# Performance work log

Hardware: AMD Instinct MI355X
Metric: run time of the kernel (lower is better)

Reference implementation:

```python
import jax, jax.numpy as jnp
import numpy as np

P, Q = 8, 8  # patch_size


def _patchify(x):
    # x: [b, c, H, W] -> patches [b, h*w, c*p*q]
    b, c, H, W = x.shape
    h, w = H // P, W // Q
    x = x.reshape(b, c, h, P, w, Q)
    x = x.transpose(0, 2, 4, 1, 3, 5)  # b h w c p q
    return x.reshape(b, h * w, c * P * Q)


def _depatchify(patches, c, H, W):
    # patches: [b, h*w, c*p*q] -> [b, c, H, W]
    b = patches.shape[0]
    h, w = H // P, W // Q
    x = patches.reshape(b, h, w, c, P, Q)
    x = x.transpose(0, 3, 1, 4, 2, 5)  # b c h p w q
    return x.reshape(b, c, H, W)


def setup_inputs() -> dict:
    key = jax.random.key(0)
    x = jax.random.normal(key, (16, 3, 512, 512), dtype=jnp.float32)
    return {"x": x, "rank": 32}


def reference(x, rank):
    b, c, H, W = x.shape
    patches = _patchify(x)  # [b, N, D] with N = (H/8)*(W/8), D = c*64
    u, s, vt = jnp.linalg.svd(patches, full_matrices=False)
    u = u[..., :rank]          # [b, N, r]
    s = s[..., :rank]          # [b, r]
    vt = vt[..., :rank, :]     # [b, r, D]
    # original: u*sqrt(s), v = sqrt(s)*vt^T; reconstruction u @ v^T == (u*s) @ vt
    recon = (u * s[..., None, :]) @ vt  # [b, N, D]
    return _depatchify(recon, c, H, W)
```

## Files before the change

### kernel.cpp

```cpp
#include <hip/hip_runtime.h>
#include <cstdint>
#include <cstddef>

#define IMG 512
#define JD 192

__device__ inline float fast_rcp(float x) { return __builtin_amdgcn_rcpf(x); }

__global__ __launch_bounds__(256) void k_gram(const float* __restrict__ x,
                                              float* __restrict__ part) {
  const int ck = blockIdx.x;
  const int sl = blockIdx.y;
  const int b  = blockIdx.z;
  const int t  = threadIdx.x;
  __shared__ float tile[32][JD];
  const int ty = t >> 5;
  const int tx = t & 31;
  const int r0 = sl*48 + ty*6;
  const int c0 = tx*6;
  float acc[6][6];
#pragma unroll
  for (int i=0;i<6;i++)
#pragma unroll
    for (int j=0;j<6;j++) acc[i][j]=0.f;
// ... 69 lines not shown
      const int row = f >> 5, kk = f & 31;
      Ar[row][kk] = Sb[(ti*64+row)*JD + k0+kk];
      Br[row][kk] = Sb[(tj*64+row)*JD + k0+kk];
    }
    __syncthreads();
#pragma unroll 4
    for (int k=0;k<32;k++) {
      float va[4], vb[4];
#pragma unroll
      for (int i=0;i<4;i++) va[i] = Ar[ty*4+i][k];
#pragma unroll
      for (int j=0;j<4;j++) vb[j] = Br[tx*4+j][k];
#pragma unroll
      for (int i=0;i<4;i++)
#pragma unroll
        for (int j=0;j<4;j++) acc[i][j] += va[i]*vb[j];
    }
    __syncthreads();
  }
#pragma unroll
  for (int i=0;i<4;i++)
#pragma unroll
    for (int j=0;j<4;j++) {
      const int r = ti*64+ty*4+i, c = tj*64+tx*4+j;
      Db[r*JD+c] = acc[i][j];
      if (ti != tj) Db[c*JD+r] = acc[i][j];
    }
}


__device__ void orth_lds(float* __restrict__ Wl, float* __restrict__ S1,
                         float* __restrict__ rdv, float* __restrict__ pdv,
                         float* __restrict__ misc, int t, float ridge) {
  const int ty = t >> 4, tx = t & 15;
  float acc[4][4];
#pragma unroll
  for (int i=0;i<4;i++)
#pragma unroll
    for (int j=0;j<4;j++) acc[i][j]=0.f;
  __syncthreads();
#pragma unroll 2
  for (int r=0; r<JD; r++) {
    const float4 va4 = *(const float4*)(Wl + r*68 + ty*4);
    const float4 vb4 = *(const float4*)(Wl + r*68 + tx*4);
    const float a4[4] = {va4.x, va4.y, va4.z, va4.w};
    const float b4[4] = {vb4.x, vb4.y, vb4.z, vb4.w};
#pragma unroll
    for (int i=0;i<4;i++)
#pragma unroll
      for (int j=0;j<4;j++) acc[i][j] += a4[i]*b4[j];
  }
#pragma unroll
  for (int i=0;i<4;i++)
#pragma unroll
    for (int j=0;j<4;j++)
      S1[(ty*4+i)*68 + tx*4+j] = acc[i][j];
  __syncthreads();
  if (ridge > 0.f) {
    if (t < 64) {
      float d = S1[t*68+t];
#pragma unroll
      for (int o=1;o<64;o<<=1) d = fmaxf(d, __shfl_xor(d, o));
      if (t == 0) misc[0] = d * ridge;
    }
    __syncthreads();
    if (t < 64) S1[t*68+t] += misc[0];
    __syncthreads();
  }
  for (int p=0; p<4; p++) {
    const int b16 = p*16;
    if (t < 64) {
      for (int jj=0; jj<16; jj++) {
        const int j = b16 + jj;
        const float invd = fast_rcp(S1[j*68+j]);
        if (t == 0) pdv[jj] = invd;
        const int nit = (15-jj)*16;
        for (int f=t; f<nit; f+=64) {
          const int i = j+1 + (f>>4);
          const int k = j+1 + (f&15);
          if (k <= i)
            S1[i*68+k] -= S1[i*68+j]*S1[k*68+j]*invd;
        }
      }
    }
    __syncthreads();
    const int rb = b16 + 16;
    if (t < 64 - rb) {
      const int r = rb + t;
      float pr[16];
      float4* prp = (float4*)pr;
      prp[0] = *(const float4*)(S1 + r*68 + b16);
      prp[1] = *(const float4*)(S1 + r*68 + b16 + 4);
      prp[2] = *(const float4*)(S1 + r*68 + b16 + 8);
      prp[3] = *(const float4*)(S1 + r*68 + b16 + 12);
#pragma unroll
      for (int c=1; c<16; c++) {
        float s = pr[c];
#pragma unroll
        for (int j=0; j<c; j++) s -= pr[j]*S1[(b16+c)*68 + b16+j]*pdv[j];
        pr[c] = s;
      }
      *(float4*)(S1 + r*68 + b16)      = prp[0];
      *(float4*)(S1 + r*68 + b16 + 4)  = prp[1];
      *(float4*)(S1 + r*68 + b16 + 8)  = prp[2];
      *(float4*)(S1 + r*68 + b16 + 12) = prp[3];
    }
    __syncthreads();
    for (int f=t; f<2304; f+=256) {
      const int i = rb + f/48;
      const int k = rb + (f - (f/48)*48);
      if (i < 64 && k < 64 && k <= i) {
        float s = S1[i*68+k];
#pragma unroll
        for (int jj=0; jj<16; jj++)
          s -= S1[i*68 + b16+jj]*S1[k*68 + b16+jj]*pdv[jj];
        S1[i*68+k] = s;
      }
    }
    __syncthreads();
  }
  if (t < 64) rdv[t] = rsqrtf(S1[t*68+t]);
  __syncthreads();
  for (int f=t; f<4096; f+=256) {
    const int i = f>>6, k = f&63;
    if (k < i) S1[i*68+k] *= rdv[k];
  }
  __syncthreads();
  if (t < JD) {
    float w[64];
    float4* wp = (float4*)w;
#pragma unroll
    for (int c4=0;c4<16;c4++) wp[c4] = *(const float4*)(Wl + t*68 + c4*4);
#pragma unroll
    for (int c=0;c<64;c++) {
      float v = w[c];
#pragma unroll
      for (int k=0;k<c;k++) v -= w[k]*S1[c*68+k];
      w[c] = v * rdv[c];
    }
#pragma unroll
    for (int c4=0;c4<16;c4++) *(float4*)(Wl + t*68 + c4*4) = wp[c4];
  }
  __syncthreads();
}

__device__ void mm_lds(const float* __restrict__ G, const float* __restrict__ Win,
                       float* __restrict__ Wout, float* __restrict__ Gt, int t) {
  const int rg = t >> 2, cg = t & 3;
  float acc[3][16];
#pragma unroll
  for (int i=0;i<3;i++)
#pragma unroll
    for (int j=0;j<16;j++) acc[i][j]=0.f;
  for (int k0=0; k0<JD; k0+=32) {
    __syncthreads();
    for (int f=t; f<6144; f+=256) {
      const int r = f >> 5, kk = f & 31;
      Gt[kk*193 + r] = G[r*JD + k0 + kk];
    }
    __syncthreads();
#pragma unroll 2
    for (int k=0;k<32;k++) {
      const float a0 = Gt[k*193 + rg*3+0];
      const float a1 = Gt[k*193 + rg*3+1];
      const float a2 = Gt[k*193 + rg*3+2];
      const float* wr = Win + (k0+k)*68 + cg*16;
#pragma unroll
      for (int j4=0;j4<4;j4++) {
        const float4 b4 = *(const float4*)(wr + 4*j4);
        const float bb[4] = {b4.x, b4.y, b4.z, b4.w};
#pragma unroll
        for (int jj=0;jj<4;jj++) {
          acc[0][j4*4+jj] += a0*bb[jj];
          acc[1][j4*4+jj] += a1*bb[jj];
          acc[2][j4*4+jj] += a2*bb[jj];
        }
      }
    }
  }
  __syncthreads();
#pragma unroll
  for (int i=0;i<3;i++)
#pragma unroll
    for (int j=0;j<16;j++)
      Wout[(rg*3+i)*68 + cg*16 + j] = acc[i][j];
  __syncthreads();
}

__device__ void hgemm_lds(const float* __restrict__ X, const float* __restrict__ Y,
                          float* __restrict__ S1, int t) {
  const int ty = t >> 4, tx = t & 15;
  float acc[4][4];
#pragma unroll
  for (int i=0;i<4;i++)
#pragma unroll
    for (int j=0;j<4;j++) acc[i][j]=0.f;
#pragma unroll 2
  for (int r=0; r<JD; r++) {
    const float4 va4 = *(const float4*)(X + r*68 + ty*4);
    const float4 vb4 = *(const float4*)(Y + r*68 + tx*4);
    const float a4[4] = {va4.x, va4.y, va4.z, va4.w};
    const float b4[4] = {vb4.x, vb4.y, vb4.z, vb4.w};
#pragma unroll
    for (int i=0;i<4;i++)
#pragma unroll
      for (int j=0;j<4;j++) acc[i][j] += a4[i]*b4[j];
  }
  __syncthreads();
#pragma unroll
  for (int i=0;i<4;i++)
#pragma unroll
    for (int j=0;j<4;j++)
      S1[(ty*4+i)*68 + tx*4+j] = acc[i][j];
  __syncthreads();
}

__global__ __launch_bounds__(256) void k_sub(const float* __restrict__ G32g,
                                             const float* __restrict__ Gsg,
                                             float* __restrict__ WbG,
                                             float* __restrict__ Hgg) {
  const int b = blockIdx.x;
  const int t = threadIdx.x;
  __shared__ float W0l[192*68];
  __shared__ float W1l[192*68];
  __shared__ float scr[32*193];
  __shared__ float rdv[64];
  __shared__ float pdv[16];
  __shared__ float misc[8];
  const float* Gb  = G32g + (size_t)b*JD*JD;
  const float* Gsb = Gsg  + (size_t)b*JD*JD;

  for (int f=t; f<JD*64; f+=256)
    W0l[(f>>6)*68 + (f&63)] = Gb[(f>>6)*JD + (f&63)];
  __syncthreads();

  orth_lds(W0l, scr, rdv, pdv, misc, t, 1e-6f);
  mm_lds(Gb, W0l, W1l, scr, t);
  orth_lds(W1l, scr, rdv, pdv, misc, t, 1e-6f);
  orth_lds(W1l, scr, rdv, pdv, misc, t, 0.f);

  mm_lds(Gsb, W1l, W0l, scr, t);
  hgemm_lds(W1l, W0l, scr, t);

  float* Wb = WbG + (size_t)b*JD*64;
  for (int f=t; f<JD*64; f+=256)
    Wb[f] = W1l[(f>>6)*68 + (f&63)];
  float* Hb = Hgg + (size_t)b*64*68;
  for (int f=t; f<64*68; f+=256) Hb[f] = scr[f];
}

__device__ void dev_tridiag(float* __restrict__ A, float* a, float* b2,
                            float* bsg, float* v0s, float* bts,
                            float* vvec, float* wvec, int t) {
  for (int j=0; j<=61; j++) {
    const int m = 63 - j;
    if (t < 64) {
      float xi = (t < m) ? A[j*68 + (j+1+t)] : 0.f;
      float nr = xi*xi;
#pragma unroll
      for (int o=1;o<64;o<<=1) nr += __shfl_xor(nr, o);
      const float sig = sqrtf(nr);
      const float alpha = __shfl(xi, 0);
      const float sgn = (alpha >= 0.f) ? 1.f : -1.f;
      const float v0 = alpha + sgn*sig;
      const float beta = (sig > 1e-20f) ? 1.0f/(sig*fabsf(v0)) : 0.f;
      if (t < m) vvec[t] = (t==0) ? v0 : xi;
      if (t == 0) {
        a[j] = A[j*68+j]; b2[j] = nr; bsg[j] = -sgn*sig;
        v0s[j] = v0; bts[j] = beta;
      }
      float pv = 0.f;
      if (t < m) {
        const float* row = A + (j+1+t)*68 + (j+1);
        for (int c=0;c<m;c++) pv += row[c]*vvec[c];
        pv *= beta;
      }
      float dp = (t<m) ? vvec[t]*pv : 0.f;
#pragma unroll
      for (int o=1;o<64;o<<=1) dp += __shfl_xor(dp, o);
      const float gamma = 0.5f*beta*dp;
      if (t < m) wvec[t] = pv - gamma*vvec[t];
    }
    __syncthreads();
    const int mm = m*m;
    for (int f=t; f<mm; f+=256) {
      const int r = f/m, c = f - r*m;
      A[(j+1+r)*68 + (j+1+c)] -= vvec[r]*wvec[c] + wvec[r]*vvec[c];
    }
    __syncthreads();
  }
  if (t == 0) {
    a[62] = A[62*68+62];
    a[63] = A[63*68+63];
    const float bb = A[62*68+63];
    b2[62] = bb*bb;
    bsg[62] = bb;
  }
  __syncthreads();
}

__device__ inline int sturm_cnt_fast(const float* a, const float* b2, float sig) {
  float d = a[0] - sig;
  int n = (d < 0.f) ? 1 : 0;
#pragma unroll 8
  for (int i=1;i<64;i++) {
    const float dd = (fabsf(d) < 1e-20f) ? -1e-20f : d;
    d = (a[i]-sig) - b2[i-1]*fast_rcp(dd);
    n += (d < 0.f) ? 1 : 0;
  }
  return n;
}

__device__ inline float dguard(float d) {
  if (fabsf(d) < 1e-12f) return (d < 0.f) ? -1e-12f : 1e-12f;
  return d;
}

__global__ __launch_bounds__(256) void k_tri(float* __restrict__ Hgg,
                                             float* __restrict__ vec5) {
  const int b = blockIdx.x;
  const int t = threadIdx.x;
  __shared__ float SH[64*68];
  __shared__ float a64[64];
  __shared__ float b2v[64];
  __shared__ float bsg[64];
  __shared__ float v0s[64];
  __shared__ float bts[64];
  __shared__ float vvec[64];
  __shared__ float wvec[64];
  float* Hb = Hgg + (size_t)b*64*68;
  for (int f=t; f<64*68; f+=256) SH[f] = Hb[f];
  __syncthreads();
  dev_tridiag(SH, a64, b2v, bsg, v0s, bts, vvec, wvec, t);
  for (int f=t; f<64*68; f+=256) Hb[f] = SH[f];
  float* vb = vec5 + (size_t)b*320;
  if (t < 64) {
    vb[t]     = a64[t];
    vb[64+t]  = b2v[t];
    vb[128+t] = bsg[t];
    vb[192+t] = v0s[t];
    vb[256+t] = bts[t];
  }
}

__global__ __launch_bounds__(256) void k_vec(const float* __restrict__ Hgg,
                                             const float* __restrict__ vec5,
                                             float* __restrict__ VtG) {
  const int b = blockIdx.x;
  const int t = threadIdx.x;
  __shared__ float SH[64*68];
  __shared__ float Vt[64*36];
  __shared__ float dpA[64*33];
  __shared__ float dmA[64*33];
  __shared__ float ps[8*33];
  __shared__ float wvred[32];
  __shared__ float rdv[64];
  __shared__ float a64[64];
  __shared__ float b2v[64];
  __shared__ float bsg[64];
  __shared__ float v0s[64];
  __shared__ float bts[64];
  __shared__ float lam[32];
  __shared__ float misc[8];
  const float* Hb = Hgg + (size_t)b*64*68;
  const float* vb = vec5 + (size_t)b*320;
  for (int f=t; f<64*68; f+=256) SH[f] = Hb[f];
  if (t < 64) {
    a64[t] = vb[t];
    b2v[t] = vb[64+t];
    bsg[t] = vb[128+t];
    v0s[t] = vb[192+t];
    bts[t] = vb[256+t];
  }
  __syncthreads();

  if (t < 64) {
    const float bl = (t>0)  ? sqrtf(b2v[t-1]) : 0.f;
    const float br = (t<63) ? sqrtf(b2v[t])   : 0.f;
    float lo = a64[t] - bl - br, hi = a64[t] + bl + br;
#pragma unroll
    for (int o=1;o<64;o<<=1) {
      lo = fminf(lo, __shfl_xor(lo,o));
      hi = fmaxf(hi, __shfl_xor(hi,o));
    }
    if (t == 0) { misc[0] = lo - 1e-4f; misc[1] = hi + 1e-4f; }
  }
  __syncthreads();

  {
    const int l = t >> 3, g = t & 7;
    const int r = 32 + l;
    float L = misc[0], H = misc[1];
    for (int it=0; it<10; it++) {
      const float mid = L + (H-L)*((float)(g+1)*(1.0f/9.0f));
      const int cnt = sturm_cnt_fast(a64, b2v, mid);
      float nL = L, nH = H;
#pragma unroll
      for (int k=0;k<8;k++) {
        const int ck = __shfl(cnt, k, 8);
        const float pk = L + (H-L)*((float)(k+1)*(1.0f/9.0f));
        if (ck <= r) nL = fmaxf(nL, pk); else nH = fminf(nH, pk);
      }
      L = nL; H = nH;
    }
    if (g == 0) lam[l] = 0.5f*(L+H);
  }
  __syncthreads();
// ... 62 lines not shown
        dpA[i*33+k] -= dpA[i*33+j]*dpA[k*33+j]*invd;
    }
  }
  __syncthreads();
  if (t < 32) rdv[t] = rsqrtf(dpA[t*33+t]);
  __syncthreads();
  for (int f=t; f<1024; f+=256) {
    const int i = f>>5, k = f&31;
    if (k < i) dpA[i*33+k] *= rdv[k];
  }
  __syncthreads();
  if (t < 64) {
    float w[32];
#pragma unroll
    for (int c=0;c<32;c++) w[c] = Vt[t*36+c];
#pragma unroll
    for (int c=0;c<32;c++) {
      float v = w[c];
#pragma unroll
      for (int k=0;k<c;k++) v -= w[k]*dpA[c*33+k];
      w[c] = v * rdv[c];
    }
#pragma unroll
    for (int c=0;c<32;c++) Vt[t*36+c] = w[c];
  }
  __syncthreads();

  for (int j=61; j>=0; j--) {
    const int m = 63 - j;
    {
      const int c = t & 31, g = t >> 5;
      float s = 0.f;
      for (int r=g; r<m; r+=8) {
        const float vr = (r==0) ? v0s[j] : SH[j*68 + (j+1+r)];
        s += vr * Vt[(j+1+r)*36 + c];
      }
      ps[g*33+c] = s;
    }
    __syncthreads();
    if (t < 32) {
      float s = 0.f;
#pragma unroll
      for (int g=0;g<8;g++) s += ps[g*33+t];
      wvred[t] = s * bts[j];
    }
    __syncthreads();
    {
      const int c = t & 31, g = t >> 5;
      for (int r=g; r<m; r+=8) {
        const float vr = (r==0) ? v0s[j] : SH[j*68 + (j+1+r)];
        Vt[(j+1+r)*36 + c] -= vr * wvred[c];
      }
    }
    __syncthreads();
  }

  float* Vb = VtG + (size_t)b*2048;
  for (int f=t; f<2048; f+=256) Vb[f] = Vt[(f>>5)*36 + (f&31)];
}

__global__ __launch_bounds__(256) void k_bm(const float* __restrict__ WbG,
                                            const float* __restrict__ VtG,
                                            float* __restrict__ Mg) {
  const int b = blockIdx.x;
  const int t = threadIdx.x;
  __shared__ float Vt[64*36];
  __shared__ float Bt[32*196];
  const float* W = WbG + (size_t)b*JD*64;
  const float* Vb = VtG + (size_t)b*2048;
  float* Mb = Mg + (size_t)b*JD*JD;
  for (int f=t; f<2048; f+=256) Vt[(f>>5)*36 + (f&31)] = Vb[f];
  __syncthreads();

  if (t < JD) {
    float accv[32];
#pragma unroll
    for (int c=0;c<32;c++) accv[c] = 0.f;
    const float4* crow = (const float4*)(W + t*64);
#pragma unroll 2
    for (int kb=0; kb<16; kb++) {
      const float4 av = crow[kb];
      const float a4[4] = {av.x, av.y, av.z, av.w};
#pragma unroll
      for (int ki=0; ki<4; ki++) {
        const float aa = a4[ki];
        const float* vrow = Vt + (kb*4+ki)*36;
        const float4 v0 = *(const float4*)(vrow+0);
        const float4 v1 = *(const float4*)(vrow+4);
        const float4 v2 = *(const float4*)(vrow+8);
        const float4 v3 = *(const float4*)(vrow+12);
        const float4 v4 = *(const float4*)(vrow+16);
        const float4 v5 = *(const float4*)(vrow+20);
        const float4 v6 = *(const float4*)(vrow+24);
        const float4 v7 = *(const float4*)(vrow+28);
        accv[0]+=aa*v0.x; accv[1]+=aa*v0.y; accv[2]+=aa*v0.z; accv[3]+=aa*v0.w;
        accv[4]+=aa*v1.x; accv[5]+=aa*v1.y; accv[6]+=aa*v1.z; accv[7]+=aa*v1.w;
        accv[8]+=aa*v2.x; accv[9]+=aa*v2.y; accv[10]+=aa*v2.z; accv[11]+=aa*v2.w;
        accv[12]+=aa*v3.x; accv[13]+=aa*v3.y; accv[14]+=aa*v3.z; accv[15]+=aa*v3.w;
        accv[16]+=aa*v4.x; accv[17]+=aa*v4.y; accv[18]+=aa*v4.z; accv[19]+=aa*v4.w;
        accv[20]+=aa*v5.x; accv[21]+=aa*v5.y; accv[22]+=aa*v5.z; accv[23]+=aa*v5.w;
        accv[24]+=aa*v6.x; accv[25]+=aa*v6.y; accv[26]+=aa*v6.z; accv[27]+=aa*v6.w;
        accv[28]+=aa*v7.x; accv[29]+=aa*v7.y; accv[30]+=aa*v7.z; accv[31]+=aa*v7.w;
      }
    }
#pragma unroll
    for (int c=0;c<32;c++) Bt[c*196 + t] = accv[c];
  }
  __syncthreads();

  for (int tt=t; tt<576; tt+=256) {
    const int tr = tt/24, tc = tt - tr*24;
    const int r0 = tr*8, c0 = tc*8;
    float acc2[8][8];
#pragma unroll
    for (int i=0;i<8;i++)
#pragma unroll
      for (int j=0;j<8;j++) acc2[i][j]=0.f;
    for (int k=0;k<32;k++) {
      const float* br = Bt + k*196;
      const float4 a0 = *(const float4*)(br + r0);
      const float4 a1 = *(const float4*)(br + r0 + 4);
      const float4 b0 = *(const float4*)(br + c0);
      const float4 b1 = *(const float4*)(br + c0 + 4);
      const float va[8] = {a0.x,a0.y,a0.z,a0.w,a1.x,a1.y,a1.z,a1.w};
      const float vb[8] = {b0.x,b0.y,b0.z,b0.w,b1.x,b1.y,b1.z,b1.w};
#pragma unroll
      for (int i=0;i<8;i++)
#pragma unroll
        for (int j=0;j<8;j++) acc2[i][j] += va[i]*vb[j];
    }
#pragma unroll
    for (int i=0;i<8;i++)
#pragma unroll
      for (int j=0;j<8;j++)
        Mb[(r0+i)*JD + c0+j] = acc2[i][j];
  }
}

__global__ __launch_bounds__(256) void k_recon(const float* __restrict__ x,
                                               const float* __restrict__ Mg,
                                               float* __restrict__ out) {
  const int nb = blockIdx.x;
  const int b  = blockIdx.y;
  const int t  = threadIdx.x;
  __shared__ float At[32][17];
  __shared__ float Mt[16][JD];
  const float* xb = x + (size_t)b*3*IMG*IMG;
  const float* Mb = Mg + (size_t)b*JD*JD;
  float* ob = out + (size_t)b*3*IMG*IMG;
  const int pg = t >> 4;
  const int jg = t & 15;
  float acc[2][12];
#pragma unroll
  for (int i=0;i<2;i++)
#pragma unroll
    for (int j=0;j<12;j++) acc[i][j]=0.f;
  for (int j0=0; j0<JD; j0+=16) {
    for (int f=t; f<512; f+=256) {
      const int nl = f >> 4, jj = f & 15;
      const int j = j0 + jj;
      const int n = nb*32 + nl;
      const int hh = n >> 6, ww = n & 63;
      const int c = j >> 6, p = (j >> 3) & 7, q = j & 7;
      At[nl][jj] = xb[(c*IMG + hh*8+p)*IMG + ww*8 + q];
    }
    for (int f=t; f<3072; f+=256) {
      const int jj = f / JD, cc = f - jj*JD;
      Mt[jj][cc] = Mb[(j0+jj)*JD + cc];
    }
    __syncthreads();
#pragma unroll 4
    for (int jj=0;jj<16;jj++) {
      const float a0 = At[pg*2+0][jj];
      const float a1 = At[pg*2+1][jj];
#pragma unroll
      for (int j=0;j<12;j++) {
        const float mm = Mt[jj][jg*12+j];
        acc[0][j] += a0*mm;
        acc[1][j] += a1*mm;
      }
    }
    __syncthreads();
  }
#pragma unroll
  for (int i=0;i<2;i++) {
    const int n = nb*32 + pg*2 + i;
    const int hh = n >> 6, ww = n & 63;
#pragma unroll
    for (int j4=0;j4<3;j4++) {
      const int jo = jg*12 + j4*4;
      const int c = jo >> 6, p = (jo >> 3) & 7, q = jo & 7;
      const float4 v = make_float4(acc[i][j4*4+0], acc[i][j4*4+1],
                                   acc[i][j4*4+2], acc[i][j4*4+3]);
      *(float4*)(ob + (size_t)(c*IMG + hh*8+p)*IMG + ww*8 + q) = v;
    }
  }
}

extern "C" void kernel_launch(void* const* d_in, const int* in_sizes, int n_in,
                              void* d_out, int out_size, void* d_ws, size_t ws_size,
                              hipStream_t stream) {
  (void)in_sizes; (void)n_in; (void)out_size; (void)ws_size;
  const float* x = (const float*)d_in[0];
  float* out = (float*)d_out;
  float* ws  = (float*)d_ws;

  float* part = ws;
  float* Gs   = ws + 2359296;
  float* P0   = ws + 2949120;
  float* P1   = ws + 3538944;
  float* Mg   = ws;
  float* Wb   = ws + 786432;
  float* Hg   = ws + 983040;
  float* v5   = ws + 1052672;
  float* Vtg  = ws + 1057792;

  k_gram  <<<dim3(4,4,16), 256, 0, stream>>>(x, part);
  k_greduce<<<2304,        256, 0, stream>>>(part, Gs);
  k_sq    <<<dim3(6,16),   256, 0, stream>>>(Gs, P0);
  k_sq    <<<dim3(6,16),   256, 0, stream>>>(P0, P1);
  k_sq    <<<dim3(6,16),   256, 0, stream>>>(P1, P0);
  k_sq    <<<dim3(6,16),   256, 0, stream>>>(P0, P1);
  k_sq    <<<dim3(6,16),   256, 0, stream>>>(P1, P0);
  k_sub   <<<16,           256, 0, stream>>>(P0, Gs, Wb, Hg);
  k_tri   <<<16,           256, 0, stream>>>(Hg, v5);
  k_vec   <<<16,           256, 0, stream>>>(Hg, v5, Vtg);
  k_bm    <<<16,           256, 0, stream>>>(Wb, Vtg, Mg);
  k_recon <<<dim3(128,16), 256, 0, stream>>>(x, Mg, out);
}
```

Before: 952.0 us.

## Widen k_sub to 1024 threads with smaller per-thread GEMM tiles

Launches the per-batch subspace-iteration kernel k_sub with 1024 threads instead of 256 and remaps its LDS GEMMs (Gram, mm, hgemm) to 2x2 or 3x4 per-thread tiles. Strided loops now step by 1024. The triangular-solve step of orth_lds now works directly on the LDS row instead of copying it into a 64-float register array. The goal is more parallelism in a kernel that runs only 16 blocks. The risks are less reuse per thread, more LDS traffic, and slower LDS access in the forward solve. Some sections, such as the Cholesky panel step guarded by t<64 and the t<JD solve, may not be written to use the extra threads.

Result: slower. 1.060 ms (+11.4%).

```diff
diff --git a/kernel.cpp b/kernel.cpp
--- a/kernel.cpp
+++ b/kernel.cpp
@@ -125,29 +125,20 @@
 __device__ void orth_lds(float* __restrict__ Wl, float* __restrict__ S1,
                          float* __restrict__ rdv, float* __restrict__ pdv,
                          float* __restrict__ misc, int t, float ridge) {
-  const int ty = t >> 4, tx = t & 15;
-  float acc[4][4];
-#pragma unroll
-  for (int i=0;i<4;i++)
-#pragma unroll
-    for (int j=0;j<4;j++) acc[i][j]=0.f;
-  __syncthreads();
-#pragma unroll 2
+  const int ty = t >> 5, tx = t & 31;
+  float a00=0.f, a01=0.f, a10=0.f, a11=0.f;
+  __syncthreads();
+#pragma unroll 4
   for (int r=0; r<JD; r++) {
-    const float4 va4 = *(const float4*)(Wl + r*68 + ty*4);
-    const float4 vb4 = *(const float4*)(Wl + r*68 + tx*4);
-    const float a4[4] = {va4.x, va4.y, va4.z, va4.w};
-    const float b4[4] = {vb4.x, vb4.y, vb4.z, vb4.w};
-#pragma unroll
-    for (int i=0;i<4;i++)
-#pragma unroll
-      for (int j=0;j<4;j++) acc[i][j] += a4[i]*b4[j];
-  }
-#pragma unroll
-  for (int i=0;i<4;i++)
-#pragma unroll
-    for (int j=0;j<4;j++)
-      S1[(ty*4+i)*68 + tx*4+j] = acc[i][j];
+    const float2 va = *(const float2*)(Wl + r*68 + ty*2);
+    const float2 vb = *(const float2*)(Wl + r*68 + tx*2);
+    a00 += va.x*vb.x; a01 += va.x*vb.y;
+    a10 += va.y*vb.x; a11 += va.y*vb.y;
+  }
+  S1[(ty*2+0)*68 + tx*2+0] = a00;
+  S1[(ty*2+0)*68 + tx*2+1] = a01;
+  S1[(ty*2+1)*68 + tx*2+0] = a10;
+  S1[(ty*2+1)*68 + tx*2+1] = a11;
   __syncthreads();
   if (ridge > 0.f) {
     if (t < 64) {
@@ -199,7 +190,7 @@
       *(float4*)(S1 + r*68 + b16 + 12) = prp[3];
     }
     __syncthreads();
-    for (int f=t; f<2304; f+=256) {
+    for (int f=t; f<2304; f+=1024) {
       const int i = rb + f/48;
       const int k = rb + (f - (f/48)*48);
       if (i < 64 && k < 64 && k <= i) {
@@ -214,60 +205,50 @@
   }
   if (t < 64) rdv[t] = rsqrtf(S1[t*68+t]);
   __syncthreads();
-  for (int f=t; f<4096; f+=256) {
+  for (int f=t; f<4096; f+=1024) {
     const int i = f>>6, k = f&63;
     if (k < i) S1[i*68+k] *= rdv[k];
   }
   __syncthreads();
   if (t < JD) {
-    float w[64];
-    float4* wp = (float4*)w;
-#pragma unroll
-    for (int c4=0;c4<16;c4++) wp[c4] = *(const float4*)(Wl + t*68 + c4*4);
-#pragma unroll
+    float* wr = Wl + t*68;
     for (int c=0;c<64;c++) {
-      float v = w[c];
-#pragma unroll
-      for (int k=0;k<c;k++) v -= w[k]*S1[c*68+k];
-      w[c] = v * rdv[c];
-    }
-#pragma unroll
-    for (int c4=0;c4<16;c4++) *(float4*)(Wl + t*68 + c4*4) = wp[c4];
+      float v = wr[c];
+      for (int k=0;k<c;k++) v -= wr[k]*S1[c*68+k];
+      wr[c] = v * rdv[c];
+    }
   }
   __syncthreads();
 }
 
 __device__ void mm_lds(const float* __restrict__ G, const float* __restrict__ Win,
                        float* __restrict__ Wout, float* __restrict__ Gt, int t) {
-  const int rg = t >> 2, cg = t & 3;
-  float acc[3][16];
+  const int rg = t >> 4;
+  const int cg = t & 15;
+  float acc[3][4];
 #pragma unroll
   for (int i=0;i<3;i++)
 #pragma unroll
-    for (int j=0;j<16;j++) acc[i][j]=0.f;
+    for (int j=0;j<4;j++) acc[i][j]=0.f;
   for (int k0=0; k0<JD; k0+=32) {
     __syncthreads();
-    for (int f=t; f<6144; f+=256) {
+    for (int f=t; f<6144; f+=1024) {
       const int r = f >> 5, kk = f & 31;
       Gt[kk*193 + r] = G[r*JD + k0 + kk];
     }
     __syncthreads();
-#pragma unroll 2
+#pragma unroll 4
     for (int k=0;k<32;k++) {
       const float a0 = Gt[k*193 + rg*3+0];
       const float a1 = Gt[k*193 + rg*3+1];
       const float a2 = Gt[k*193 + rg*3+2];
-      const float* wr = Win + (k0+k)*68 + cg*16;
-#pragma unroll
-      for (int j4=0;j4<4;j4++) {
-        const float4 b4 = *(const float4*)(wr + 4*j4);
-        const float bb[4] = {b4.x, b4.y, b4.z, b4.w};
-#pragma unroll
-        for (int jj=0;jj<4;jj++) {
-          acc[0][j4*4+jj] += a0*bb[jj];
-          acc[1][j4*4+jj] += a1*bb[jj];
-          acc[2][j4*4+jj] += a2*bb[jj];
-        }
+      const float4 b4 = *(const float4*)(Win + (k0+k)*68 + cg*4);
+      const float bb[4] = {b4.x, b4.y, b4.z, b4.w};
+#pragma unroll
+      for (int jj=0;jj<4;jj++) {
+        acc[0][jj] += a0*bb[jj];
+        acc[1][jj] += a1*bb[jj];
+        acc[2][jj] += a2*bb[jj];
       }
     }
   }
@@ -275,43 +256,34 @@
 #pragma unroll
   for (int i=0;i<3;i++)
 #pragma unroll
-    for (int j=0;j<16;j++)
-      Wout[(rg*3+i)*68 + cg*16 + j] = acc[i][j];
+    for (int j=0;j<4;j++)
+      Wout[(rg*3+i)*68 + cg*4 + j] = acc[i][j];
   __syncthreads();
 }
 
 __device__ void hgemm_lds(const float* __restrict__ X, const float* __restrict__ Y,
                           float* __restrict__ S1, int t) {
-  const int ty = t >> 4, tx = t & 15;
-  float acc[4][4];
-#pragma unroll
-  for (int i=0;i<4;i++)
-#pragma unroll
-    for (int j=0;j<4;j++) acc[i][j]=0.f;
-#pragma unroll 2
+  const int ty = t >> 5, tx = t & 31;
+  float a00=0.f, a01=0.f, a10=0.f, a11=0.f;
+#pragma unroll 4
   for (int r=0; r<JD; r++) {
-    const float4 va4 = *(const float4*)(X + r*68 + ty*4);
-    const float4 vb4 = *(const float4*)(Y + r*68 + tx*4);
-    const float a4[4] = {va4.x, va4.y, va4.z, va4.w};
-    const float b4[4] = {vb4.x, vb4.y, vb4.z, vb4.w};
-#pragma unroll
-    for (int i=0;i<4;i++)
-#pragma unroll
-      for (int j=0;j<4;j++) acc[i][j] += a4[i]*b4[j];
-  }
-  __syncthreads();
-#pragma unroll
-  for (int i=0;i<4;i++)
-#pragma unroll
-    for (int j=0;j<4;j++)
-      S1[(ty*4+i)*68 + tx*4+j] = acc[i][j];
-  __syncthreads();
-}
-
-__global__ __launch_bounds__(256) void k_sub(const float* __restrict__ G32g,
-                                             const float* __restrict__ Gsg,
-                                             float* __restrict__ WbG,
-                                             float* __restrict__ Hgg) {
+    const float2 va = *(const float2*)(X + r*68 + ty*2);
+    const float2 vb = *(const float2*)(Y + r*68 + tx*2);
+    a00 += va.x*vb.x; a01 += va.x*vb.y;
+    a10 += va.y*vb.x; a11 += va.y*vb.y;
+  }
+  __syncthreads();
+  S1[(ty*2+0)*68 + tx*2+0] = a00;
+  S1[(ty*2+0)*68 + tx*2+1] = a01;
+  S1[(ty*2+1)*68 + tx*2+0] = a10;
+  S1[(ty*2+1)*68 + tx*2+1] = a11;
+  __syncthreads();
+}
+
+__global__ __launch_bounds__(1024) void k_sub(const float* __restrict__ G32g,
+                                              const float* __restrict__ Gsg,
+                                              float* __restrict__ WbG,
+                                              float* __restrict__ Hgg) {
   const int b = blockIdx.x;
   const int t = threadIdx.x;
   __shared__ float W0l[192*68];
@@ -323,7 +295,7 @@
   const float* Gb  = G32g + (size_t)b*JD*JD;
   const float* Gsb = Gsg  + (size_t)b*JD*JD;
 
-  for (int f=t; f<JD*64; f+=256)
+  for (int f=t; f<JD*64; f+=1024)
     W0l[(f>>6)*68 + (f&63)] = Gb[(f>>6)*JD + (f&63)];
   __syncthreads();
 
@@ -336,10 +308,10 @@
   hgemm_lds(W1l, W0l, scr, t);
 
   float* Wb = WbG + (size_t)b*JD*64;
-  for (int f=t; f<JD*64; f+=256)
+  for (int f=t; f<JD*64; f+=1024)
     Wb[f] = W1l[(f>>6)*68 + (f&63)];
   float* Hb = Hgg + (size_t)b*64*68;
-  for (int f=t; f<64*68; f+=256) Hb[f] = scr[f];
+  for (int f=t; f<64*68; f+=1024) Hb[f] = scr[f];
 }
 
 __device__ void dev_tridiag(float* __restrict__ A, float* a, float* b2,
@@ -777,16 +749,16 @@
   float* v5   = ws + 1052672;
   float* Vtg  = ws + 1057792;
 
-  k_gram  <<<dim3(4,4,16), 256, 0, stream>>>(x, part);
-  k_greduce<<<2304,        256, 0, stream>>>(part, Gs);
-  k_sq    <<<dim3(6,16),   256, 0, stream>>>(Gs, P0);
-  k_sq    <<<dim3(6,16),   256, 0, stream>>>(P0, P1);
-  k_sq    <<<dim3(6,16),   256, 0, stream>>>(P1, P0);
-  k_sq    <<<dim3(6,16),   256, 0, stream>>>(P0, P1);
-  k_sq    <<<dim3(6,16),   256, 0, stream>>>(P1, P0);
-  k_sub   <<<16,           256, 0, stream>>>(P0, Gs, Wb, Hg);
-  k_tri   <<<16,           256, 0, stream>>>(Hg, v5);
-  k_vec   <<<16,           256, 0, stream>>>(Hg, v5, Vtg);
-  k_bm    <<<16,           256, 0, stream>>>(Wb, Vtg, Mg);
-  k_recon <<<dim3(128,16), 256, 0, stream>>>(x, Mg, out);
-}
+  k_gram  <<<dim3(4,4,16), 256,  0, stream>>>(x, part);
+  k_greduce<<<2304,        256,  0, stream>>>(part, Gs);
+  k_sq    <<<dim3(6,16),   256,  0, stream>>>(Gs, P0);
+  k_sq    <<<dim3(6,16),   256,  0, stream>>>(P0, P1);
+  k_sq    <<<dim3(6,16),   256,  0, stream>>>(P1, P0);
+  k_sq    <<<dim3(6,16),   256,  0, stream>>>(P0, P1);
+  k_sq    <<<dim3(6,16),   256,  0, stream>>>(P1, P0);
+  k_sub   <<<16,           1024, 0, stream>>>(P0, Gs, Wb, Hg);
+  k_tri   <<<16,           256,  0, stream>>>(Hg, v5);
+  k_vec   <<<16,           256,  0, stream>>>(Hg, v5, Vtg);
+  k_bm    <<<16,           256,  0, stream>>>(Wb, Vtg, Mg);
+  k_recon <<<dim3(128,16), 256,  0, stream>>>(x, Mg, out);
+}
```

## Fuse subspace, tridiagonalization, eigenvector, and projection kernels into one

Applied to the files above, without the earlier changes.

Merges the four per-batch eigen-pipeline kernels (subspace iteration, tridiagonalization, eigenvector computation, projection matrix build) into a single kernel that keeps the intermediates in aliased shared memory instead of writing them to global memory. This removes three kernel launches and the global round trips for W, H, the tridiagonal vectors and Vt. It also vectorizes the M tile loads and reads in the reconstruction kernel with float4. The shared-buffer aliasing is fragile: Bt now uses a 193 stride, so float4 accesses at k*193 may be misaligned.

Measured after the change: 983.2 us. +3.3%, slower.

```diff
diff --git a/kernel.cpp b/kernel.cpp
--- a/kernel.cpp
+++ b/kernel.cpp
@@ -308,10 +308,76 @@
   __syncthreads();
 }
 
-__global__ __launch_bounds__(256) void k_sub(const float* __restrict__ G32g,
-                                             const float* __restrict__ Gsg,
-                                             float* __restrict__ WbG,
-                                             float* __restrict__ Hgg) {
+__device__ void dev_tridiag(float* __restrict__ A, float* a, float* b2,
+                            float* bsg, float* v0s, float* bts,
+                            float* vvec, float* wvec, int t) {
+  for (int j=0; j<=61; j++) {
+    const int m = 63 - j;
+    if (t < 64) {
+      float xi = (t < m) ? A[j*68 + (j+1+t)] : 0.f;
+      float nr = xi*xi;
+#pragma unroll
+      for (int o=1;o<64;o<<=1) nr += __shfl_xor(nr, o);
+      const float sig = sqrtf(nr);
+      const float alpha = __shfl(xi, 0);
+      const float sgn = (alpha >= 0.f) ? 1.f : -1.f;
+      const float v0 = alpha + sgn*sig;
+      const float beta = (sig > 1e-20f) ? 1.0f/(sig*fabsf(v0)) : 0.f;
+      if (t < m) vvec[t] = (t==0) ? v0 : xi;
+      if (t == 0) {
+        a[j] = A[j*68+j]; b2[j] = nr; bsg[j] = -sgn*sig;
+        v0s[j] = v0; bts[j] = beta;
+      }
+      float pv = 0.f;
+      if (t < m) {
+        const float* row = A + (j+1+t)*68 + (j+1);
+        for (int c=0;c<m;c++) pv += row[c]*vvec[c];
+        pv *= beta;
+      }
+      float dp = (t<m) ? vvec[t]*pv : 0.f;
+#pragma unroll
+      for (int o=1;o<64;o<<=1) dp += __shfl_xor(dp, o);
+      const float gamma = 0.5f*beta*dp;
+      if (t < m) wvec[t] = pv - gamma*vvec[t];
+    }
+    __syncthreads();
+    const int mm = m*m;
+    for (int f=t; f<mm; f+=256) {
+      const int r = f/m, c = f - r*m;
+      A[(j+1+r)*68 + (j+1+c)] -= vvec[r]*wvec[c] + wvec[r]*vvec[c];
+    }
+    __syncthreads();
+  }
+  if (t == 0) {
+    a[62] = A[62*68+62];
+    a[63] = A[63*68+63];
+    const float bb = A[62*68+63];
+    b2[62] = bb*bb;
+    bsg[62] = bb;
+  }
+  __syncthreads();
+}
+
+__device__ inline int sturm_cnt_fast(const float* a, const float* b2, float sig) {
+  float d = a[0] - sig;
+  int n = (d < 0.f) ? 1 : 0;
+#pragma unroll 8
+  for (int i=1;i<64;i++) {
+    const float dd = (fabsf(d) < 1e-20f) ? -1e-20f : d;
+    d = (a[i]-sig) - b2[i-1]*fast_rcp(dd);
+    n += (d < 0.f) ? 1 : 0;
+  }
+  return n;
+}
+
+__device__ inline float dguard(float d) {
+  if (fabsf(d) < 1e-12f) return (d < 0.f) ? -1e-12f : 1e-12f;
+  return d;
+}
+
+__global__ __launch_bounds__(256) void k_eigall(const float* __restrict__ G32g,
+                                                const float* __restrict__ Gsg,
+                                                float* __restrict__ Mg) {
   const int b = blockIdx.x;
   const int t = threadIdx.x;
   __shared__ float W0l[192*68];
@@ -322,11 +388,11 @@
   __shared__ float misc[8];
   const float* Gb  = G32g + (size_t)b*JD*JD;
   const float* Gsb = Gsg  + (size_t)b*JD*JD;
+  float* Mb = Mg + (size_t)b*JD*JD;
 
   for (int f=t; f<JD*64; f+=256)
     W0l[(f>>6)*68 + (f&63)] = Gb[(f>>6)*JD + (f&63)];
   __syncthreads();
-
   orth_lds(W0l, scr, rdv, pdv, misc, t, 1e-6f);
   mm_lds(Gb, W0l, W1l, scr, t);
   orth_lds(W1l, scr, rdv, pdv, misc, t, 1e-6f);
@@ -335,137 +401,22 @@
   mm_lds(Gsb, W1l, W0l, scr, t);
   hgemm_lds(W1l, W0l, scr, t);
 
-  float* Wb = WbG + (size_t)b*JD*64;
-  for (int f=t; f<JD*64; f+=256)
-    Wb[f] = W1l[(f>>6)*68 + (f&63)];
-  float* Hb = Hgg + (size_t)b*64*68;
-  for (int f=t; f<64*68; f+=256) Hb[f] = scr[f];
-}
-
-__device__ void dev_tridiag(float* __restrict__ A, float* a, float* b2,
-                            float* bsg, float* v0s, float* bts,
-                            float* vvec, float* wvec, int t) {
-  for (int j=0; j<=61; j++) {
-    const int m = 63 - j;
-    if (t < 64) {
-      float xi = (t < m) ? A[j*68 + (j+1+t)] : 0.f;
-      float nr = xi*xi;
-#pragma unroll
-      for (int o=1;o<64;o<<=1) nr += __shfl_xor(nr, o);
-      const float sig = sqrtf(nr);
-      const float alpha = __shfl(xi, 0);
-      const float sgn = (alpha >= 0.f) ? 1.f : -1.f;
-      const float v0 = alpha + sgn*sig;
-      const float beta = (sig > 1e-20f) ? 1.0f/(sig*fabsf(v0)) : 0.f;
-      if (t < m) vvec[t] = (t==0) ? v0 : xi;
-      if (t == 0) {
-        a[j] = A[j*68+j]; b2[j] = nr; bsg[j] = -sgn*sig;
-        v0s[j] = v0; bts[j] = beta;
-      }
-      float pv = 0.f;
-      if (t < m) {
-        const float* row = A + (j+1+t)*68 + (j+1);
-        for (int c=0;c<m;c++) pv += row[c]*vvec[c];
-        pv *= beta;
-      }
-      float dp = (t<m) ? vvec[t]*pv : 0.f;
-#pragma unroll
-      for (int o=1;o<64;o<<=1) dp += __shfl_xor(dp, o);
-      const float gamma = 0.5f*beta*dp;
-      if (t < m) wvec[t] = pv - gamma*vvec[t];
-    }
-    __syncthreads();
-    const int mm = m*m;
-    for (int f=t; f<mm; f+=256) {
-      const int r = f/m, c = f - r*m;
-      A[(j+1+r)*68 + (j+1+c)] -= vvec[r]*wvec[c] + wvec[r]*vvec[c];
-    }
-    __syncthreads();
-  }
-  if (t == 0) {
-    a[62] = A[62*68+62];
-    a[63] = A[63*68+63];
-    const float bb = A[62*68+63];
-    b2[62] = bb*bb;
-    bsg[62] = bb;
-  }
-  __syncthreads();
-}
-
-__device__ inline int sturm_cnt_fast(const float* a, const float* b2, float sig) {
-  float d = a[0] - sig;
-  int n = (d < 0.f) ? 1 : 0;
-#pragma unroll 8
-  for (int i=1;i<64;i++) {
-    const float dd = (fabsf(d) < 1e-20f) ? -1e-20f : d;
-    d = (a[i]-sig) - b2[i-1]*fast_rcp(dd);
-    n += (d < 0.f) ? 1 : 0;
-  }
-  return n;
-}
-
-__device__ inline float dguard(float d) {
-  if (fabsf(d) < 1e-12f) return (d < 0.f) ? -1e-12f : 1e-12f;
-  return d;
-}
-
-__global__ __launch_bounds__(256) void k_tri(float* __restrict__ Hgg,
-                                             float* __restrict__ vec5) {
-  const int b = blockIdx.x;
-  const int t = threadIdx.x;
-  __shared__ float SH[64*68];
-  __shared__ float a64[64];
-  __shared__ float b2v[64];
-  __shared__ float bsg[64];
-  __shared__ float v0s[64];
-  __shared__ float bts[64];
-  __shared__ float vvec[64];
-  __shared__ float wvec[64];
-  float* Hb = Hgg + (size_t)b*64*68;
-  for (int f=t; f<64*68; f+=256) SH[f] = Hb[f];
-  __syncthreads();
+  float* SH   = scr;
+  float* a64  = scr + 4352;
+  float* b2v  = scr + 4416;
+  float* bsg  = scr + 4480;
+  float* v0s  = scr + 4544;
+  float* bts  = scr + 4608;
+  float* vvec = scr + 4672;
+  float* wvec = scr + 4736;
+  float* Vt    = W0l;
+  float* dpA   = W0l + 2304;
+  float* dmA   = W0l + 4416;
+  float* ps    = W0l + 6528;
+  float* lam   = W0l + 6792;
+  float* wvred = W0l + 6824;
+
   dev_tridiag(SH, a64, b2v, bsg, v0s, bts, vvec, wvec, t);
-  for (int f=t; f<64*68; f+=256) Hb[f] = SH[f];
-  float* vb = vec5 + (size_t)b*320;
-  if (t < 64) {
-    vb[t]     = a64[t];
-    vb[64+t]  = b2v[t];
-    vb[128+t] = bsg[t];
-    vb[192+t] = v0s[t];
-    vb[256+t] = bts[t];
-  }
-}
-
-__global__ __launch_bounds__(256) void k_vec(const float* __restrict__ Hgg,
-                                             const float* __restrict__ vec5,
-                                             float* __restrict__ VtG) {
-  const int b = blockIdx.x;
-  const int t = threadIdx.x;
-  __shared__ float SH[64*68];
-  __shared__ float Vt[64*36];
-  __shared__ float dpA[64*33];
-  __shared__ float dmA[64*33];
-  __shared__ float ps[8*33];
-  __shared__ float wvred[32];
-  __shared__ float rdv[64];
-  __shared__ float a64[64];
-  __shared__ float b2v[64];
-  __shared__ float bsg[64];
-  __shared__ float v0s[64];
-  __shared__ float bts[64];
-  __shared__ float lam[32];
-  __shared__ float misc[8];
-  const float* Hb = Hgg + (size_t)b*64*68;
-  const float* vb = vec5 + (size_t)b*320;
-  for (int f=t; f<64*68; f+=256) SH[f] = Hb[f];
-  if (t < 64) {
-    a64[t] = vb[t];
-    b2v[t] = vb[64+t];
-    bsg[t] = vb[128+t];
-    v0s[t] = vb[192+t];
-    bts[t] = vb[256+t];
-  }
-  __syncthreads();
 
   if (t < 64) {
     const float bl = (t>0)  ? sqrtf(b2v[t-1]) : 0.f;
@@ -617,28 +568,13 @@
     __syncthreads();
   }
 
-  float* Vb = VtG + (size_t)b*2048;
-  for (int f=t; f<2048; f+=256) Vb[f] = Vt[(f>>5)*36 + (f&31)];
-}
-
-__global__ __launch_bounds__(256) void k_bm(const float* __restrict__ WbG,
-                                            const float* __restrict__ VtG,
-                                            float* __restrict__ Mg) {
-  const int b = blockIdx.x;
-  const int t = threadIdx.x;
-  __shared__ float Vt[64*36];
-  __shared__ float Bt[32*196];
-  const float* W = WbG + (size_t)b*JD*64;
-  const float* Vb = VtG + (size_t)b*2048;
-  float* Mb = Mg + (size_t)b*JD*JD;
-  for (int f=t; f<2048; f+=256) Vt[(f>>5)*36 + (f&31)] = Vb[f];
-  __syncthreads();
-
+  float* Bt = scr;
+  __syncthreads();
   if (t < JD) {
     float accv[32];
 #pragma unroll
     for (int c=0;c<32;c++) accv[c] = 0.f;
-    const float4* crow = (const float4*)(W + t*64);
+    const float4* crow = (const float4*)(W1l + t*68);
 #pragma unroll 2
     for (int kb=0; kb<16; kb++) {
       const float4 av = crow[kb];
@@ -666,7 +602,7 @@
       }
     }
 #pragma unroll
-    for (int c=0;c<32;c++) Bt[c*196 + t] = accv[c];
+    for (int c=0;c<32;c++) Bt[c*193 + t] = accv[c];
   }
   __syncthreads();
 
@@ -679,7 +615,7 @@
 #pragma unroll
       for (int j=0;j<8;j++) acc2[i][j]=0.f;
     for (int k=0;k<32;k++) {
-      const float* br = Bt + k*196;
+      const float* br = Bt + k*193;
       const float4 a0 = *(const float4*)(br + r0);
       const float4 a1 = *(const float4*)(br + r0 + 4);
       const float4 b0 = *(const float4*)(br + c0);
@@ -726,20 +662,24 @@
       const int c = j >> 6, p = (j >> 3) & 7, q = j & 7;
       At[nl][jj] = xb[(c*IMG + hh*8+p)*IMG + ww*8 + q];
     }
-    for (int f=t; f<3072; f+=256) {
-      const int jj = f / JD, cc = f - jj*JD;
-      Mt[jj][cc] = Mb[(j0+jj)*JD + cc];
+    for (int f=t; f<768; f+=256) {
+      const int jj = f/48, cc = (f - jj*48)*4;
+      *(float4*)(&Mt[jj][cc]) = *(const float4*)(Mb + (size_t)(j0+jj)*JD + cc);
     }
     __syncthreads();
 #pragma unroll 4
     for (int jj=0;jj<16;jj++) {
       const float a0 = At[pg*2+0][jj];
       const float a1 = At[pg*2+1][jj];
+      const float4 m0 = *(const float4*)(&Mt[jj][jg*12]);
+      const float4 m1 = *(const float4*)(&Mt[jj][jg*12+4]);
+      const float4 m2 = *(const float4*)(&Mt[jj][jg*12+8]);
+      const float mm[12] = {m0.x,m0.y,m0.z,m0.w,m1.x,m1.y,m1.z,m1.w,
+                            m2.x,m2.y,m2.z,m2.w};
 #pragma unroll
       for (int j=0;j<12;j++) {
-        const float mm = Mt[jj][jg*12+j];
-        acc[0][j] += a0*mm;
-        acc[1][j] += a1*mm;
+        acc[0][j] += a0*mm[j];
+        acc[1][j] += a1*mm[j];
       }
     }
     __syncthreads();
@@ -772,10 +712,6 @@
   float* P0   = ws + 2949120;
   float* P1   = ws + 3538944;
   float* Mg   = ws;
-  float* Wb   = ws + 786432;
-  float* Hg   = ws + 983040;
-  float* v5   = ws + 1052672;
-  float* Vtg  = ws + 1057792;
 
   k_gram  <<<dim3(4,4,16), 256, 0, stream>>>(x, part);
   k_greduce<<<2304,        256, 0, stream>>>(part, Gs);
@@ -784,9 +720,6 @@
   k_sq    <<<dim3(6,16),   256, 0, stream>>>(P1, P0);
   k_sq    <<<dim3(6,16),   256, 0, stream>>>(P0, P1);
   k_sq    <<<dim3(6,16),   256, 0, stream>>>(P1, P0);
-  k_sub   <<<16,           256, 0, stream>>>(P0, Gs, Wb, Hg);
-  k_tri   <<<16,           256, 0, stream>>>(Hg, v5);
-  k_vec   <<<16,           256, 0, stream>>>(Hg, v5, Vtg);
-  k_bm    <<<16,           256, 0, stream>>>(Wb, Vtg, Mg);
+  k_eigall<<<16,           256, 0, stream>>>(P0, Gs, Mg);
   k_recon <<<dim3(128,16), 256, 0, stream>>>(x, Mg, out);
 }
```

## Split final B·Bᵀ product into parallel symmetric-tile kernel and pad H stride

Applied to the files above, without the earlier changes.

The per-batch kernel that built M = B·Bᵀ on a single block is split in two. One kernel computes B and writes it to workspace, and a new kernel computes M over 6 lower-triangular 64x64 tiles per batch, mirroring the off-diagonal tiles, so 96 blocks run instead of 16. The 64x64 H matrix stride changes from 68 to 65 to reduce LDS bank conflicts in the tridiagonalization. The reconstruction kernel now loads and reads M tiles with float4 accesses. The cost is one extra launch and a global round-trip for B.

New measurement: 982.9 us. 1.03x slower.

```diff
diff --git a/kernel.cpp b/kernel.cpp
--- a/kernel.cpp
+++ b/kernel.cpp
@@ -281,7 +281,7 @@
 }
 
 __device__ void hgemm_lds(const float* __restrict__ X, const float* __restrict__ Y,
-                          float* __restrict__ S1, int t) {
+                          float* __restrict__ S1, int ss, int t) {
   const int ty = t >> 4, tx = t & 15;
   float acc[4][4];
 #pragma unroll
@@ -304,14 +304,14 @@
   for (int i=0;i<4;i++)
 #pragma unroll
     for (int j=0;j<4;j++)
-      S1[(ty*4+i)*68 + tx*4+j] = acc[i][j];
-  __syncthreads();
-}
-
-__global__ __launch_bounds__(256) void k_sub(const float* __restrict__ G32g,
-                                             const float* __restrict__ Gsg,
-                                             float* __restrict__ WbG,
-                                             float* __restrict__ Hgg) {
+      S1[(ty*4+i)*ss + tx*4+j] = acc[i][j];
+  __syncthreads();
+}
+
+__global__ __launch_bounds__(256) void k_subH(const float* __restrict__ G32g,
+                                              const float* __restrict__ Gsg,
+                                              float* __restrict__ WbG,
+                                              float* __restrict__ Hgg) {
   const int b = blockIdx.x;
   const int t = threadIdx.x;
   __shared__ float W0l[192*68];
@@ -333,13 +333,13 @@
   orth_lds(W1l, scr, rdv, pdv, misc, t, 0.f);
 
   mm_lds(Gsb, W1l, W0l, scr, t);
-  hgemm_lds(W1l, W0l, scr, t);
+  hgemm_lds(W1l, W0l, scr, 65, t);
 
   float* Wb = WbG + (size_t)b*JD*64;
   for (int f=t; f<JD*64; f+=256)
     Wb[f] = W1l[(f>>6)*68 + (f&63)];
-  float* Hb = Hgg + (size_t)b*64*68;
-  for (int f=t; f<64*68; f+=256) Hb[f] = scr[f];
+  float* Hb = Hgg + (size_t)b*4160;
+  for (int f=t; f<4160; f+=256) Hb[f] = scr[f];
 }
 
 __device__ void dev_tridiag(float* __restrict__ A, float* a, float* b2,
@@ -348,7 +348,7 @@
   for (int j=0; j<=61; j++) {
     const int m = 63 - j;
     if (t < 64) {
-      float xi = (t < m) ? A[j*68 + (j+1+t)] : 0.f;
+      float xi = (t < m) ? A[j*65 + (j+1+t)] : 0.f;
       float nr = xi*xi;
 #pragma unroll
       for (int o=1;o<64;o<<=1) nr += __shfl_xor(nr, o);
@@ -359,12 +359,12 @@
       const float beta = (sig > 1e-20f) ? 1.0f/(sig*fabsf(v0)) : 0.f;
       if (t < m) vvec[t] = (t==0) ? v0 : xi;
       if (t == 0) {
-        a[j] = A[j*68+j]; b2[j] = nr; bsg[j] = -sgn*sig;
+        a[j] = A[j*65+j]; b2[j] = nr; bsg[j] = -sgn*sig;
         v0s[j] = v0; bts[j] = beta;
       }
       float pv = 0.f;
       if (t < m) {
-        const float* row = A + (j+1+t)*68 + (j+1);
+        const float* row = A + (j+1+t)*65 + (j+1);
         for (int c=0;c<m;c++) pv += row[c]*vvec[c];
         pv *= beta;
       }
@@ -378,18 +378,45 @@
     const int mm = m*m;
     for (int f=t; f<mm; f+=256) {
       const int r = f/m, c = f - r*m;
-      A[(j+1+r)*68 + (j+1+c)] -= vvec[r]*wvec[c] + wvec[r]*vvec[c];
+      A[(j+1+r)*65 + (j+1+c)] -= vvec[r]*wvec[c] + wvec[r]*vvec[c];
     }
     __syncthreads();
   }
   if (t == 0) {
-    a[62] = A[62*68+62];
-    a[63] = A[63*68+63];
-    const float bb = A[62*68+63];
+    a[62] = A[62*65+62];
+    a[63] = A[63*65+63];
+    const float bb = A[62*65+63];
     b2[62] = bb*bb;
     bsg[62] = bb;
   }
   __syncthreads();
+}
+
+__global__ __launch_bounds__(256) void k_trid(float* __restrict__ Hgg,
+                                              float* __restrict__ vec5) {
+  const int b = blockIdx.x;
+  const int t = threadIdx.x;
+  __shared__ float SH[4160];
+  __shared__ float a64[64];
+  __shared__ float b2v[64];
+  __shared__ float bsg[64];
+  __shared__ float v0s[64];
+  __shared__ float bts[64];
+  __shared__ float vvec[64];
+  __shared__ float wvec[64];
+  float* Hb = Hgg + (size_t)b*4160;
+  for (int f=t; f<4160; f+=256) SH[f] = Hb[f];
+  __syncthreads();
+  dev_tridiag(SH, a64, b2v, bsg, v0s, bts, vvec, wvec, t);
+  for (int f=t; f<4160; f+=256) Hb[f] = SH[f];
+  float* vb = vec5 + (size_t)b*320;
+  if (t < 64) {
+    vb[t]     = a64[t];
+    vb[64+t]  = b2v[t];
+    vb[128+t] = bsg[t];
+    vb[192+t] = v0s[t];
+    vb[256+t] = bts[t];
+  }
 }
 
 __device__ inline int sturm_cnt_fast(const float* a, const float* b2, float sig) {
@@ -409,39 +436,12 @@
   return d;
 }
 
-__global__ __launch_bounds__(256) void k_tri(float* __restrict__ Hgg,
-                                             float* __restrict__ vec5) {
-  const int b = blockIdx.x;
-  const int t = threadIdx.x;
-  __shared__ float SH[64*68];
-  __shared__ float a64[64];
-  __shared__ float b2v[64];
-  __shared__ float bsg[64];
-  __shared__ float v0s[64];
-  __shared__ float bts[64];
-  __shared__ float vvec[64];
-  __shared__ float wvec[64];
-  float* Hb = Hgg + (size_t)b*64*68;
-  for (int f=t; f<64*68; f+=256) SH[f] = Hb[f];
-  __syncthreads();
-  dev_tridiag(SH, a64, b2v, bsg, v0s, bts, vvec, wvec, t);
-  for (int f=t; f<64*68; f+=256) Hb[f] = SH[f];
-  float* vb = vec5 + (size_t)b*320;
-  if (t < 64) {
-    vb[t]     = a64[t];
-    vb[64+t]  = b2v[t];
-    vb[128+t] = bsg[t];
-    vb[192+t] = v0s[t];
-    vb[256+t] = bts[t];
-  }
-}
-
 __global__ __launch_bounds__(256) void k_vec(const float* __restrict__ Hgg,
                                              const float* __restrict__ vec5,
                                              float* __restrict__ VtG) {
   const int b = blockIdx.x;
   const int t = threadIdx.x;
-  __shared__ float SH[64*68];
+  __shared__ float SH[4160];
   __shared__ float Vt[64*36];
   __shared__ float dpA[64*33];
   __shared__ float dmA[64*33];
@@ -455,9 +455,9 @@
   __shared__ float bts[64];
   __shared__ float lam[32];
   __shared__ float misc[8];
-  const float* Hb = Hgg + (size_t)b*64*68;
+  const float* Hb = Hgg + (size_t)b*4160;
   const float* vb = vec5 + (size_t)b*320;
-  for (int f=t; f<64*68; f+=256) SH[f] = Hb[f];
+  for (int f=t; f<4160; f+=256) SH[f] = Hb[f];
   if (t < 64) {
     a64[t] = vb[t];
     b2v[t] = vb[64+t];
@@ -594,7 +594,7 @@
       const int c = t & 31, g = t >> 5;
       float s = 0.f;
       for (int r=g; r<m; r+=8) {
-        const float vr = (r==0) ? v0s[j] : SH[j*68 + (j+1+r)];
+        const float vr = (r==0) ? v0s[j] : SH[j*65 + (j+1+r)];
         s += vr * Vt[(j+1+r)*36 + c];
       }
       ps[g*33+c] = s;
@@ -610,7 +610,7 @@
     {
       const int c = t & 31, g = t >> 5;
       for (int r=g; r<m; r+=8) {
-        const float vr = (r==0) ? v0s[j] : SH[j*68 + (j+1+r)];
+        const float vr = (r==0) ? v0s[j] : SH[j*65 + (j+1+r)];
         Vt[(j+1+r)*36 + c] -= vr * wvred[c];
       }
     }
@@ -621,19 +621,17 @@
   for (int f=t; f<2048; f+=256) Vb[f] = Vt[(f>>5)*36 + (f&31)];
 }
 
-__global__ __launch_bounds__(256) void k_bm(const float* __restrict__ WbG,
+__global__ __launch_bounds__(256) void k_bv(const float* __restrict__ WbG,
                                             const float* __restrict__ VtG,
-                                            float* __restrict__ Mg) {
+                                            float* __restrict__ Btg) {
   const int b = blockIdx.x;
   const int t = threadIdx.x;
   __shared__ float Vt[64*36];
-  __shared__ float Bt[32*196];
   const float* W = WbG + (size_t)b*JD*64;
   const float* Vb = VtG + (size_t)b*2048;
-  float* Mb = Mg + (size_t)b*JD*JD;
+  float* Bt = Btg + (size_t)b*32*JD;
   for (int f=t; f<2048; f+=256) Vt[(f>>5)*36 + (f&31)] = Vb[f];
   __syncthreads();
-
   if (t < JD) {
     float accv[32];
 #pragma unroll
@@ -666,37 +664,54 @@
       }
     }
 #pragma unroll
-    for (int c=0;c<32;c++) Bt[c*196 + t] = accv[c];
-  }
-  __syncthreads();
-
-  for (int tt=t; tt<576; tt+=256) {
-    const int tr = tt/24, tc = tt - tr*24;
-    const int r0 = tr*8, c0 = tc*8;
-    float acc2[8][8];
-#pragma unroll
-    for (int i=0;i<8;i++)
-#pragma unroll
-      for (int j=0;j<8;j++) acc2[i][j]=0.f;
-    for (int k=0;k<32;k++) {
-      const float* br = Bt + k*196;
-      const float4 a0 = *(const float4*)(br + r0);
-      const float4 a1 = *(const float4*)(br + r0 + 4);
-      const float4 b0 = *(const float4*)(br + c0);
-      const float4 b1 = *(const float4*)(br + c0 + 4);
-      const float va[8] = {a0.x,a0.y,a0.z,a0.w,a1.x,a1.y,a1.z,a1.w};
-      const float vb[8] = {b0.x,b0.y,b0.z,b0.w,b1.x,b1.y,b1.z,b1.w};
-#pragma unroll
-      for (int i=0;i<8;i++)
-#pragma unroll
-        for (int j=0;j<8;j++) acc2[i][j] += va[i]*vb[j];
-    }
-#pragma unroll
-    for (int i=0;i<8;i++)
-#pragma unroll
-      for (int j=0;j<8;j++)
-        Mb[(r0+i)*JD + c0+j] = acc2[i][j];
-  }
+    for (int c=0;c<32;c++) Bt[c*JD + t] = accv[c];
+  }
+}
+
+__global__ __launch_bounds__(256) void k_mm(const float* __restrict__ Btg,
+                                            float* __restrict__ Mg) {
+  const int tp = blockIdx.x;
+  const int b  = blockIdx.y;
+  int ti, tj;
+  if      (tp==0){ti=0;tj=0;} else if (tp==1){ti=1;tj=0;}
+  else if (tp==2){ti=1;tj=1;} else if (tp==3){ti=2;tj=0;}
+  else if (tp==4){ti=2;tj=1;} else            {ti=2;tj=2;}
+  const float* Bt = Btg + (size_t)b*32*JD;
+  float* Mb = Mg + (size_t)b*JD*JD;
+  __shared__ float Ar[32][68];
+  __shared__ float Br[32][68];
+  const int t = threadIdx.x;
+  const int ty = t >> 4, tx = t & 15;
+  for (int f=t; f<2048; f+=256) {
+    const int k = f >> 6, c = f & 63;
+    Ar[k][c] = Bt[k*JD + ti*64 + c];
+    Br[k][c] = Bt[k*JD + tj*64 + c];
+  }
+  __syncthreads();
+  float acc[4][4];
+#pragma unroll
+  for (int i=0;i<4;i++)
+#pragma unroll
+    for (int j=0;j<4;j++) acc[i][j]=0.f;
+#pragma unroll 4
+  for (int k=0;k<32;k++) {
+    const float4 va4 = *(const float4*)(&Ar[k][ty*4]);
+    const float4 vb4 = *(const float4*)(&Br[k][tx*4]);
+    const float a4[4] = {va4.x, va4.y, va4.z, va4.w};
+    const float b4[4] = {vb4.x, vb4.y, vb4.z, vb4.w};
+#pragma unroll
+    for (int i=0;i<4;i++)
+#pragma unroll
+      for (int j=0;j<4;j++) acc[i][j] += a4[i]*b4[j];
+  }
+#pragma unroll
+  for (int i=0;i<4;i++)
+#pragma unroll
+    for (int j=0;j<4;j++) {
+      const int r = ti*64+ty*4+i, c = tj*64+tx*4+j;
+      Mb[r*JD+c] = acc[i][j];
+      if (ti != tj) Mb[c*JD+r] = acc[i][j];
+    }
 }
 
 __global__ __launch_bounds__(256) void k_recon(const float* __restrict__ x,
@@ -726,20 +741,24 @@
       const int c = j >> 6, p = (j >> 3) & 7, q = j & 7;
       At[nl][jj] = xb[(c*IMG + hh*8+p)*IMG + ww*8 + q];
     }
-    for (int f=t; f<3072; f+=256) {
-      const int jj = f / JD, cc = f - jj*JD;
-      Mt[jj][cc] = Mb[(j0+jj)*JD + cc];
+    for (int f=t; f<768; f+=256) {
+      const int jj = f/48, cc = (f - jj*48)*4;
+      *(float4*)(&Mt[jj][cc]) = *(const float4*)(Mb + (size_t)(j0+jj)*JD + cc);
     }
     __syncthreads();
 #pragma unroll 4
     for (int jj=0;jj<16;jj++) {
       const float a0 = At[pg*2+0][jj];
       const float a1 = At[pg*2+1][jj];
+      const float4 m0 = *(const float4*)(&Mt[jj][jg*12]);
+      const float4 m1 = *(const float4*)(&Mt[jj][jg*12+4]);
+      const float4 m2 = *(const float4*)(&Mt[jj][jg*12+8]);
+      const float mm[12] = {m0.x,m0.y,m0.z,m0.w,m1.x,m1.y,m1.z,m1.w,
+                            m2.x,m2.y,m2.z,m2.w};
 #pragma unroll
       for (int j=0;j<12;j++) {
-        const float mm = Mt[jj][jg*12+j];
-        acc[0][j] += a0*mm;
-        acc[1][j] += a1*mm;
+        acc[0][j] += a0*mm[j];
+        acc[1][j] += a1*mm[j];
       }
     }
     __syncthreads();
@@ -776,6 +795,7 @@
   float* Hg   = ws + 983040;
   float* v5   = ws + 1052672;
   float* Vtg  = ws + 1057792;
+  float* Btg  = ws + 1090560;
 
   k_gram  <<<dim3(4,4,16), 256, 0, stream>>>(x, part);
   k_greduce<<<2304,        256, 0, stream>>>(part, Gs);
@@ -784,9 +804,10 @@
   k_sq    <<<dim3(6,16),   256, 0, stream>>>(P1, P0);
   k_sq    <<<dim3(6,16),   256, 0, stream>>>(P0, P1);
   k_sq    <<<dim3(6,16),   256, 0, stream>>>(P1, P0);
-  k_sub   <<<16,           256, 0, stream>>>(P0, Gs, Wb, Hg);
-  k_tri   <<<16,           256, 0, stream>>>(Hg, v5);
+  k_subH  <<<16,           256, 0, stream>>>(P0, Gs, Wb, Hg);
+  k_trid  <<<16,           256, 0, stream>>>(Hg, v5);
   k_vec   <<<16,           256, 0, stream>>>(Hg, v5, Vtg);
-  k_bm    <<<16,           256, 0, stream>>>(Wb, Vtg, Mg);
+  k_bv    <<<16,           256, 0, stream>>>(Wb, Vtg, Btg);
+  k_mm    <<<dim3(6,16),   256, 0, stream>>>(Btg, Mg);
   k_recon <<<dim3(128,16), 256, 0, stream>>>(x, Mg, out);
 }
```
